# Kernel tuning notes

Hardware: AMD Instinct MI355X
Metric: run time of the kernel (lower is better)

The kernel has to match this reference:

```python
import jax, jax.numpy as jnp
import numpy as np

RADIUS = 0.2
NSAMPLE = 32
USE_XYZ = True

B, N, NPOINT, C = 4, 16384, 2048, 64


def setup_inputs() -> dict:
    key = jax.random.key(0)
    k1, k2, k3 = jax.random.split(key, 3)
    xyz = jax.random.uniform(k1, (B, N, 3), dtype=jnp.float32)
    new_xyz = jax.random.uniform(k2, (B, NPOINT, 3), dtype=jnp.float32)
    features = jax.random.normal(k3, (B, C, N), dtype=jnp.float32)
    return {"xyz": xyz, "new_xyz": new_xyz, "features": features}


def _ball_query(radius, nsample, xyz, new_xyz):
    # xyz: (B,N,3), new_xyz: (B,S,3) -> idx: (B,S,nsample) int32
    d2 = jnp.sum((new_xyz[:, :, None, :] - xyz[:, None, :, :]) ** 2, axis=-1)  # (B,S,N)
    mask = d2 < radius * radius
    # stable sort puts in-ball indices first, preserving original order
    order = jnp.argsort(~mask, axis=-1, stable=True)  # (B,S,N)
    idx = order[..., :nsample]  # first nsample in-ball indices (or fillers)
    count = jnp.sum(mask, axis=-1, dtype=jnp.int32)  # (B,S)
    slot_valid = jnp.arange(nsample, dtype=jnp.int32)[None, None, :] < count[..., None]
    # pad with the first valid index (index 0 if the ball is empty),
    # matching the reference CUDA ball_query behavior
    idx = jnp.where(slot_valid, idx, idx[..., :1])
    return idx.astype(jnp.int32)


def _group(features, idx):
    # features: (B,C,N), idx: (B,S,K) -> (B,C,S,K)
    return jnp.take_along_axis(features[:, :, None, :], idx[:, None, :, :], axis=3)


def reference(xyz, new_xyz, features):
    idx = _ball_query(RADIUS, NSAMPLE, xyz, new_xyz)  # (B,S,K)
    xyz_t = jnp.transpose(xyz, (0, 2, 1))  # (B,3,N)
    grouped_xyz = _group(xyz_t, idx)  # (B,3,S,K)
    grouped_xyz = grouped_xyz - jnp.transpose(new_xyz, (0, 2, 1))[..., None]
    grouped_features = _group(features, idx)  # (B,C,S,K)
    if USE_XYZ:
        new_features = jnp.concatenate([grouped_xyz, grouped_features], axis=1)
    else:
        new_features = grouped_features
    return new_features  # (B, 3+C, S, K)
```

## Files before the change

### kernel.cpp

```cpp
#include <hip/hip_runtime.h>


namespace {
constexpr int kN   = 16384;
constexpr int kNP  = 2048;
constexpr int kC   = 64;
constexpr int kNS  = 32;
constexpr int kOC  = 3 + kC;
constexpr int kWin = 1024;
}

__device__ __forceinline__ float d2_rn(float nx, float ny, float nz,
                                       float px, float py, float pz) {
    const float dx = __fsub_rn(nx, px);
    const float dy = __fsub_rn(ny, py);
    const float dz = __fsub_rn(nz, pz);
    return __fadd_rn(__fadd_rn(__fmul_rn(dx, dx), __fmul_rn(dy, dy)),
                     __fmul_rn(dz, dz));
}

__global__ __launch_bounds__(256) void tr_kernel(
    const float* __restrict__ feat, float* __restrict__ tf)
{
    __shared__ float tile[64][65];
    const int b  = blockIdx.x >> 8;
    const int n0 = (blockIdx.x & 255) << 6;
    const float* fb = feat + (size_t)b * kC * kN;
    float* ob       = tf   + (size_t)b * kN * kC;
    const int t  = threadIdx.x;
    const int q  = t >> 6;
    const int nn = t & 63;
    #pragma unroll
    for (int p = 0; p < 16; ++p) {
        const int c = p * 4 + q;
        tile[c][nn] = fb[(size_t)c * kN + n0 + nn];
    }
    __syncthreads();
    const int cc = t & 63;
    #pragma unroll
    for (int p = 0; p < 16; ++p) {
        const int n = p * 4 + q;
        ob[(size_t)(n0 + n) * kC + cc] = tile[cc][n];
    }
}

__global__ __launch_bounds__(256) void qg_fused(
    const float* __restrict__ xyz,
    const float* __restrict__ new_xyz,
    const float* __restrict__ tf,
    float* __restrict__ out)
{
    __shared__ int sIdx[kNS];
    __shared__ int sTot[4];

    const int t = threadIdx.x;
    const int w = t >> 6;
    const int l = t & 63;

    const int bid = blockIdx.x;
    const int xcd = bid & 7;
    const int b   = xcd >> 1;
    const int j   = ((xcd & 1) << 10) | (bid >> 3);

    const float* __restrict__ xb = xyz + (size_t)b * kN * 3;
    const float4* __restrict__ xv = reinterpret_cast<const float4*>(xb);
    const float* nxp = new_xyz + ((size_t)b * kNP + j) * 3;
    const float nx = nxp[0], ny = nxp[1], nz = nxp[2];
    const float R2 = 0.04f;

    int count = 0;
    float4 A0, A1, A2, B0, B1, B2;
    {
        const int o = 3 * t;
        B0 = xv[o]; B1 = xv[o + 1]; B2 = xv[o + 2];
    }
    for (int base = 0; base < kN; base += kWin) {
        A0 = B0; A1 = B1; A2 = B2;
        if (base + kWin < kN) {
            const int o = ((base + kWin) >> 2) * 3 + 3 * t;
            B0 = xv[o]; B1 = xv[o + 1]; B2 = xv[o + 2];
        }
        const float d0 = d2_rn(nx, ny, nz, A0.x, A0.y, A0.z);
        const float d1 = d2_rn(nx, ny, nz, A0.w, A1.x, A1.y);
        const float d2v = d2_rn(nx, ny, nz, A1.z, A1.w, A2.x);
        const float d3 = d2_rn(nx, ny, nz, A2.y, A2.z, A2.w);
        const unsigned long long b0 = __ballot(d0 < R2);
        const unsigned long long b1 = __ballot(d1 < R2);
        const unsigned long long b2 = __ballot(d2v < R2);
        const unsigned long long b3 = __ballot(d3 < R2);

        __syncthreads();
        if (l == 0)
            sTot[w] = (int)(__popcll(b0) + __popcll(b1) +
                            __popcll(b2) + __popcll(b3));
        __syncthreads();

        int wbase = count;
        #pragma unroll
        for (int ww = 0; ww < 4; ++ww)
            if (ww < w) wbase += sTot[ww];
        const int wtot = sTot[0] + sTot[1] + sTot[2] + sTot[3];

        const unsigned long long m = (1ull << l) - 1ull;
        int slot = wbase + (int)(__popcll(b0 & m) + __popcll(b1 & m) +
                                 __popcll(b2 & m) + __popcll(b3 & m));
        const int i0 = base + 4 * t;
        if (d0 < R2)  { if (slot < kNS) sIdx[slot] = i0 + 0; ++slot; }
        if (d1 < R2)  { if (slot < kNS) sIdx[slot] = i0 + 1; ++slot; }
        if (d2v < R2) { if (slot < kNS) sIdx[slot] = i0 + 2; ++slot; }
        if (d3 < R2)  { if (slot < kNS) sIdx[slot] = i0 + 3; ++slot; }

        count += wtot;
        if (count >= kNS) break;
    }
    __syncthreads();

    if (count < kNS) {
        int fill = 0;
        if (count > 0) fill = sIdx[0];
        if (t >= count && t < kNS) sIdx[t] = fill;
    }
    __syncthreads();

    const int s = t & 31;
    const int g = t >> 5;
    const int id = sIdx[s];

    const size_t cs = (size_t)kNP * kNS;
    float* ob = out + ((size_t)b * kOC * kNP + j) * kNS + s;

    if (g == 0) {
        const float g0 = xb[(size_t)id * 3 + 0] - nx;
        const float g1 = xb[(size_t)id * 3 + 1] - ny;
        const float g2 = xb[(size_t)id * 3 + 2] - nz;
        ob[0 * cs] = g0;
        ob[1 * cs] = g1;
        ob[2 * cs] = g2;
    }

    const float* row = tf + ((size_t)b * kN + id) * kC;
    float* obf = ob + 3 * cs;
    #pragma unroll
    for (int mi = 0; mi < 2; ++mi) {
        const int mchunk = g + mi * 8;
        const float4 v = *reinterpret_cast<const float4*>(row + mchunk * 4);
        const size_t c0 = (size_t)mchunk * 4;
        obf[(c0 + 0) * cs] = v.x;
        obf[(c0 + 1) * cs] = v.y;
        obf[(c0 + 2) * cs] = v.z;
        obf[(c0 + 3) * cs] = v.w;
    }
}

__global__ __launch_bounds__(256) void qg_direct(
    const float* __restrict__ xyz, const float* __restrict__ new_xyz,
    const float* __restrict__ feat, float* __restrict__ out)
{
    __shared__ int sIdx[4][kNS];
    const int wave = threadIdx.x >> 6;
    const int lane = threadIdx.x & 63;
    const int bid  = blockIdx.x;
    const int xcd  = bid & 7;
    const int b    = xcd >> 1;
    const int jblk = ((xcd & 1) << 8) | (bid >> 3);
    const int j    = (jblk << 2) | wave;

    const float* __restrict__ xb = xyz + (size_t)b * kN * 3;
    const float* nxp = new_xyz + ((size_t)b * kNP + j) * 3;
    const float nx = nxp[0], ny = nxp[1], nz = nxp[2];
    const float R2 = 0.04f;

    int count = 0;
    for (int base = 0; base < kN; base += 64) {
        const int i = base + lane;
        const float d2 = d2_rn(nx, ny, nz, xb[(size_t)i * 3 + 0],
                               xb[(size_t)i * 3 + 1], xb[(size_t)i * 3 + 2]);
        const bool in = d2 < R2;
        const unsigned long long bal = __ballot(in);
        const int pre  = (int)__popcll(bal & ((1ull << lane) - 1ull));
        const int slot = count + pre;
        if (in && slot < kNS) sIdx[wave][slot] = i;
        count += (int)__popcll(bal);
        if (count >= kNS) break;
    }
    __builtin_amdgcn_wave_barrier();
    if (count == 0) {
        if (lane < kNS) sIdx[wave][lane] = 0;
    } else if (count < kNS) {
        const int first = sIdx[wave][0];
        __builtin_amdgcn_wave_barrier();
        if (lane >= count && lane < kNS) sIdx[wave][lane] = first;
    }
    __builtin_amdgcn_wave_barrier();

    const int s    = lane & 31;
    const int half = lane >> 5;
    const int id   = sIdx[wave][s];
    const float g0 = xb[(size_t)id * 3 + 0] - nx;
    const float g1 = xb[(size_t)id * 3 + 1] - ny;
    const float g2 = xb[(size_t)id * 3 + 2] - nz;
    const size_t cs = (size_t)kNP * kNS;
    float* ob = out + (((size_t)b * kOC) * kNP + j) * kNS + s;
    const float* fb = feat + ((size_t)b * kC) * kN + id;
    #pragma unroll
    for (int cb = 0; cb < kOC; cb += 2) {
        const int c = cb + half;
        if (c < kOC) {
            float v;
            if (c < 3) v = (c == 0) ? g0 : ((c == 1) ? g1 : g2);
            else       v = fb[(size_t)(c - 3) * kN];
            ob[(size_t)c * cs] = v;
        }
    }
}

extern "C" void kernel_launch(void* const* d_in, const int* in_sizes, int n_in,
                              void* d_out, int out_size, void* d_ws, size_t ws_size,
                              hipStream_t stream) {
    const float* xyz     = (const float*)d_in[0];
    const float* new_xyz = (const float*)d_in[1];
    const float* feat    = (const float*)d_in[2];
    float* out           = (float*)d_out;

    const size_t need = (size_t)4 * kN * kC * sizeof(float);
    if (ws_size >= need) {
        float* tf = (float*)d_ws;
        tr_kernel<<<dim3(1024), dim3(256), 0, stream>>>(feat, tf);
        qg_fused <<<dim3(8192), dim3(256), 0, stream>>>(xyz, new_xyz, tf, out);
    } else {
        qg_direct<<<dim3(2048), dim3(256), 0, stream>>>(xyz, new_xyz, feat, out);
    }
}
```

Measured before the change: 107.5 us.

## Split ball query into per-wave prep kernel fused with transpose, separate gather

Each ball query now runs in a single wave that scans 256-point windows with no block-wide syncs. The old code used one 256-thread block per query with two __syncthreads per 1024-point window. The feature transpose and the query now share one prep launch, so the two workloads can overlap, and the query writes its indices to a workspace buffer. A second gather kernel reads those indices and writes the output with four queries per block. This removes block-level synchronisation and wasted scanning past the early exit, at the cost of an extra index round-trip through global memory and a larger workspace requirement.

```diff
diff --git a/kernel.cpp b/kernel.cpp
--- a/kernel.cpp
+++ b/kernel.cpp
@@ -7,7 +7,7 @@
 constexpr int kC   = 64;
 constexpr int kNS  = 32;
 constexpr int kOC  = 3 + kC;
-constexpr int kWin = 1024;
+constexpr int kWin = 256;
 }
 
 __device__ __forceinline__ float d2_rn(float nx, float ny, float nz,
@@ -19,40 +19,107 @@
                      __fmul_rn(dz, dz));
 }
 
-__global__ __launch_bounds__(256) void tr_kernel(
-    const float* __restrict__ feat, float* __restrict__ tf)
+__global__ __launch_bounds__(256) void prep_kernel(
+    const float* __restrict__ xyz,
+    const float* __restrict__ new_xyz,
+    const float* __restrict__ feat,
+    float* __restrict__ tf,
+    int*   __restrict__ idxbuf)
 {
     __shared__ float tile[64][65];
-    const int b  = blockIdx.x >> 8;
-    const int n0 = (blockIdx.x & 255) << 6;
-    const float* fb = feat + (size_t)b * kC * kN;
-    float* ob       = tf   + (size_t)b * kN * kC;
-    const int t  = threadIdx.x;
-    const int q  = t >> 6;
-    const int nn = t & 63;
-    #pragma unroll
-    for (int p = 0; p < 16; ++p) {
-        const int c = p * 4 + q;
-        tile[c][nn] = fb[(size_t)c * kN + n0 + nn];
-    }
-    __syncthreads();
-    const int cc = t & 63;
-    #pragma unroll
-    for (int p = 0; p < 16; ++p) {
-        const int n = p * 4 + q;
-        ob[(size_t)(n0 + n) * kC + cc] = tile[cc][n];
-    }
-}
-
-__global__ __launch_bounds__(256) void qg_fused(
+    __shared__ int   sIdx[4][kNS];
+
+    const int t = threadIdx.x;
+
+    if (blockIdx.x < 1024) {
+        const int b  = blockIdx.x >> 8;
+        const int n0 = (blockIdx.x & 255) << 6;
+        const float* fb = feat + (size_t)b * kC * kN;
+        float* ob       = tf   + (size_t)b * kN * kC;
+        const int q  = t >> 6;
+        const int nn = t & 63;
+        #pragma unroll
+        for (int p = 0; p < 16; ++p) {
+            const int c = p * 4 + q;
+            tile[c][nn] = fb[(size_t)c * kN + n0 + nn];
+        }
+        __syncthreads();
+        const int cc = t & 63;
+        #pragma unroll
+        for (int p = 0; p < 16; ++p) {
+            const int n = p * 4 + q;
+            ob[(size_t)(n0 + n) * kC + cc] = tile[cc][n];
+        }
+        return;
+    }
+
+    const int w = t >> 6;
+    const int l = t & 63;
+    const int qid = (blockIdx.x - 1024) * 4 + w;
+    const int b   = qid >> 11;
+    const int j   = qid & 2047;
+
+    const float4* __restrict__ xv =
+        reinterpret_cast<const float4*>(xyz + (size_t)b * kN * 3);
+    const float* nxp = new_xyz + ((size_t)b * kNP + j) * 3;
+    const float nx = nxp[0], ny = nxp[1], nz = nxp[2];
+    const float R2 = 0.04f;
+
+    int count = 0;
+    float4 A0, A1, A2, B0, B1, B2;
+    {
+        const int o = 3 * l;
+        B0 = xv[o]; B1 = xv[o + 1]; B2 = xv[o + 2];
+    }
+    for (int base = 0; base < kN; base += kWin) {
+        A0 = B0; A1 = B1; A2 = B2;
+        if (base + kWin < kN) {
+            const int o = ((base + kWin) >> 2) * 3 + 3 * l;
+            B0 = xv[o]; B1 = xv[o + 1]; B2 = xv[o + 2];
+        }
+        const float d0  = d2_rn(nx, ny, nz, A0.x, A0.y, A0.z);
+        const float d1  = d2_rn(nx, ny, nz, A0.w, A1.x, A1.y);
+        const float d2v = d2_rn(nx, ny, nz, A1.z, A1.w, A2.x);
+        const float d3  = d2_rn(nx, ny, nz, A2.y, A2.z, A2.w);
+        const unsigned long long b0 = __ballot(d0  < R2);
+        const unsigned long long b1 = __ballot(d1  < R2);
+        const unsigned long long b2 = __ballot(d2v < R2);
+        const unsigned long long b3 = __ballot(d3  < R2);
+
+        const unsigned long long m = (1ull << l) - 1ull;
+        int slot = count + (int)(__popcll(b0 & m) + __popcll(b1 & m) +
+                                 __popcll(b2 & m) + __popcll(b3 & m));
+        const int i0 = base + 4 * l;
+        if (d0  < R2) { if (slot < kNS) sIdx[w][slot] = i0 + 0; ++slot; }
+        if (d1  < R2) { if (slot < kNS) sIdx[w][slot] = i0 + 1; ++slot; }
+        if (d2v < R2) { if (slot < kNS) sIdx[w][slot] = i0 + 2; ++slot; }
+        if (d3  < R2) { if (slot < kNS) sIdx[w][slot] = i0 + 3; ++slot; }
+
+        count += (int)(__popcll(b0) + __popcll(b1) +
+                       __popcll(b2) + __popcll(b3));
+        if (count >= kNS) break;
+    }
+    __builtin_amdgcn_wave_barrier();
+
+    if (count == 0) {
+        if (l < kNS) sIdx[w][l] = 0;
+    } else if (count < kNS) {
+        const int first = sIdx[w][0];
+        __builtin_amdgcn_wave_barrier();
+        if (l >= count && l < kNS) sIdx[w][l] = first;
+    }
+    __builtin_amdgcn_wave_barrier();
+
+    if (l < kNS) idxbuf[(size_t)qid * kNS + l] = sIdx[w][l];
+}
+
+__global__ __launch_bounds__(256) void gather_kernel(
     const float* __restrict__ xyz,
     const float* __restrict__ new_xyz,
     const float* __restrict__ tf,
+    const int*   __restrict__ idxbuf,
     float* __restrict__ out)
 {
-    __shared__ int sIdx[kNS];
-    __shared__ int sTot[4];
-
     const int t = threadIdx.x;
     const int w = t >> 6;
     const int l = t & 63;
@@ -60,76 +127,22 @@
     const int bid = blockIdx.x;
     const int xcd = bid & 7;
     const int b   = xcd >> 1;
-    const int j   = ((xcd & 1) << 10) | (bid >> 3);
+    const int jbl = ((xcd & 1) << 8) | (bid >> 3);
+    const int j   = (jbl << 2) | w;
+    const int qid = (b << 11) | j;
+
+    const int s = l & 31;
+    const int h = l >> 5;
+    const int id = idxbuf[(size_t)qid * kNS + s];
 
     const float* __restrict__ xb = xyz + (size_t)b * kN * 3;
-    const float4* __restrict__ xv = reinterpret_cast<const float4*>(xb);
     const float* nxp = new_xyz + ((size_t)b * kNP + j) * 3;
     const float nx = nxp[0], ny = nxp[1], nz = nxp[2];
-    const float R2 = 0.04f;
-
-    int count = 0;
-    float4 A0, A1, A2, B0, B1, B2;
-    {
-        const int o = 3 * t;
-        B0 = xv[o]; B1 = xv[o + 1]; B2 = xv[o + 2];
-    }
-    for (int base = 0; base < kN; base += kWin) {
-        A0 = B0; A1 = B1; A2 = B2;
-        if (base + kWin < kN) {
-            const int o = ((base + kWin) >> 2) * 3 + 3 * t;
-            B0 = xv[o]; B1 = xv[o + 1]; B2 = xv[o + 2];
-        }
-        const float d0 = d2_rn(nx, ny, nz, A0.x, A0.y, A0.z);
-        const float d1 = d2_rn(nx, ny, nz, A0.w, A1.x, A1.y);
-        const float d2v = d2_rn(nx, ny, nz, A1.z, A1.w, A2.x);
-        const float d3 = d2_rn(nx, ny, nz, A2.y, A2.z, A2.w);
-        const unsigned long long b0 = __ballot(d0 < R2);
-        const unsigned long long b1 = __ballot(d1 < R2);
-        const unsigned long long b2 = __ballot(d2v < R2);
-        const unsigned long long b3 = __ballot(d3 < R2);
-
-        __syncthreads();
-        if (l == 0)
-            sTot[w] = (int)(__popcll(b0) + __popcll(b1) +
-                            __popcll(b2) + __popcll(b3));
-        __syncthreads();
-
-        int wbase = count;
-        #pragma unroll
-        for (int ww = 0; ww < 4; ++ww)
-            if (ww < w) wbase += sTot[ww];
-        const int wtot = sTot[0] + sTot[1] + sTot[2] + sTot[3];
-
-        const unsigned long long m = (1ull << l) - 1ull;
-        int slot = wbase + (int)(__popcll(b0 & m) + __popcll(b1 & m) +
-                                 __popcll(b2 & m) + __popcll(b3 & m));
-        const int i0 = base + 4 * t;
-        if (d0 < R2)  { if (slot < kNS) sIdx[slot] = i0 + 0; ++slot; }
-        if (d1 < R2)  { if (slot < kNS) sIdx[slot] = i0 + 1; ++slot; }
-        if (d2v < R2) { if (slot < kNS) sIdx[slot] = i0 + 2; ++slot; }
-        if (d3 < R2)  { if (slot < kNS) sIdx[slot] = i0 + 3; ++slot; }
-
-        count += wtot;
-        if (count >= kNS) break;
-    }
-    __syncthreads();
-
-    if (count < kNS) {
-        int fill = 0;
-        if (count > 0) fill = sIdx[0];
-        if (t >= count && t < kNS) sIdx[t] = fill;
-    }
-    __syncthreads();
-
-    const int s = t & 31;
-    const int g = t >> 5;
-    const int id = sIdx[s];
 
     const size_t cs = (size_t)kNP * kNS;
     float* ob = out + ((size_t)b * kOC * kNP + j) * kNS + s;
 
-    if (g == 0) {
+    if (h == 0) {
         const float g0 = xb[(size_t)id * 3 + 0] - nx;
         const float g1 = xb[(size_t)id * 3 + 1] - ny;
         const float g2 = xb[(size_t)id * 3 + 2] - nz;
@@ -141,10 +154,10 @@
     const float* row = tf + ((size_t)b * kN + id) * kC;
     float* obf = ob + 3 * cs;
     #pragma unroll
-    for (int mi = 0; mi < 2; ++mi) {
-        const int mchunk = g + mi * 8;
-        const float4 v = *reinterpret_cast<const float4*>(row + mchunk * 4);
-        const size_t c0 = (size_t)mchunk * 4;
+    for (int it = 0; it < 8; ++it) {
+        const int chunk = it * 2 + h;
+        const float4 v = *reinterpret_cast<const float4*>(row + chunk * 4);
+        const size_t c0 = (size_t)chunk * 4;
         obf[(c0 + 0) * cs] = v.x;
         obf[(c0 + 1) * cs] = v.y;
         obf[(c0 + 2) * cs] = v.z;
@@ -222,11 +235,15 @@
     const float* feat    = (const float*)d_in[2];
     float* out           = (float*)d_out;
 
-    const size_t need = (size_t)4 * kN * kC * sizeof(float);
-    if (ws_size >= need) {
-        float* tf = (float*)d_ws;
-        tr_kernel<<<dim3(1024), dim3(256), 0, stream>>>(feat, tf);
-        qg_fused <<<dim3(8192), dim3(256), 0, stream>>>(xyz, new_xyz, tf, out);
+    const size_t tf_bytes  = (size_t)4 * kN * kC * sizeof(float);
+    const size_t idx_bytes = (size_t)4 * kNP * kNS * sizeof(int);
+    if (ws_size >= tf_bytes + idx_bytes) {
+        float* tf   = (float*)d_ws;
+        int* idxbuf = (int*)((char*)d_ws + tf_bytes);
+        prep_kernel  <<<dim3(3072), dim3(256), 0, stream>>>(
+            xyz, new_xyz, feat, tf, idxbuf);
+        gather_kernel<<<dim3(2048), dim3(256), 0, stream>>>(
+            xyz, new_xyz, tf, idxbuf, out);
     } else {
         qg_direct<<<dim3(2048), dim3(256), 0, stream>>>(xyz, new_xyz, feat, out);
     }
```

Measured after the change: 110.7 us. 3.0% more time.
